# Kernel optimization log

Hardware: AMD Instinct MI355X
Metric: run time of the kernel (lower is better)

The kernel has to match this reference:

```python
import jax, jax.numpy as jnp
import numpy as np

N, E = 50000, 800000
DN, DE, H = 64, 32, 4
NODE_SCALE = float(np.sqrt(DN))
EDGE_SCALE = float(np.sqrt(DE))


def _linear_init(key, fan_in, fan_out):
    k1, k2 = jax.random.split(key)
    s = 1.0 / np.sqrt(fan_in)
    w = jax.random.uniform(k1, (fan_in, fan_out), minval=-s, maxval=s, dtype=jnp.float32)
    b = jax.random.uniform(k2, (fan_out,), minval=-s, maxval=s, dtype=jnp.float32)
    return w, b


def setup_inputs() -> dict:
    key = jax.random.key(0)
    ks = jax.random.split(key, 12)
    inp = {}
    inp['node_inputs'] = jax.random.normal(ks[0], (N, DN), dtype=jnp.float32)
    inp['edge_inputs'] = jax.random.normal(ks[1], (E, DE), dtype=jnp.float32)
    inp['src'] = jax.random.randint(ks[2], (E,), 0, N, dtype=jnp.int32)
    inp['dst'] = jax.random.randint(ks[3], (E,), 0, N, dtype=jnp.int32)
    # query / key MessageProjection params, value LinearProjection params
    specs = [('qn', DN, H * DN, ks[4]), ('qe', DE, H, ks[5]),
             ('kn', DN, H * DN, ks[6]), ('ke', DE, H, ks[7]),
             ('vn', DN, H * DN, ks[8]), ('ve', DE, H * DE, ks[9])]
    for name, fi, fo, k in specs:
        w, b = _linear_init(k, fi, fo)
        inp[name + '_w'] = w
        inp[name + '_b'] = b
    return inp


def _message_proj(x, e, src, dst, nw, nb, ew, eb):
    # node projection: relu(Linear) -> [N, H, DN]; edge weight: sigmoid(Linear) -> [E, H, 1]
    p = jax.nn.relu(x @ nw + nb).reshape(-1, H, DN)
    w = jax.nn.sigmoid(e @ ew + eb).reshape(-1, H, 1)
    msg = p[src] + w  # u_add_e -> [E, H, DN]
    ssum = jax.ops.segment_sum(msg, dst, num_segments=N)
    deg = jax.ops.segment_sum(jnp.ones((E, 1, 1), msg.dtype), dst, num_segments=N)
    agg = jnp.where(deg > 0, ssum / jnp.maximum(deg, 1.0), 0.0)  # mean reduce, 0 for isolated nodes
    return agg, w


def _attention(q, k, scale):
    # scores over heads: [*, H, H]; exp -> clamp(-5,5) -> softmax (matches torch order)
    s = jnp.clip(jnp.exp(jnp.einsum('nhd,ngd->nhg', q, k) / scale), -5.0, 5.0)
    return jax.nn.softmax(s, axis=-1)


def reference(node_inputs, edge_inputs, src, dst,
              qn_w, qn_b, qe_w, qe_b, kn_w, kn_b, ke_w, ke_b,
              vn_w, vn_b, ve_w, ve_b):
    node_q, edge_q = _message_proj(node_inputs, edge_inputs, src, dst, qn_w, qn_b, qe_w, qe_b)
    node_k, edge_k = _message_proj(node_inputs, edge_inputs, src, dst, kn_w, kn_b, ke_w, ke_b)
    node_v = jax.nn.relu(node_inputs @ vn_w + vn_b).reshape(-1, H, DN)
    edge_v = jax.nn.relu(edge_inputs @ ve_w + ve_b).reshape(-1, H, DE)
    node_attn = _attention(node_q, node_k, NODE_SCALE)  # [N, H, H]
    edge_attn = _attention(edge_q, edge_k, EDGE_SCALE)  # [E, H, H]
    node_emb = jnp.einsum('nhg,ngd->nhd', node_attn, node_v).mean(-2)  # [N, DN]
    edge_emb = jnp.einsum('ehg,egd->ehd', edge_attn, edge_v).mean(-2)  # [E, DE]
    return node_emb, edge_emb
```

## Files before the change

kernel.cpp:

```cpp
#include <hip/hip_runtime.h>
#include <math.h>

#define NN 50000
#define NE 800000

__device__ __forceinline__ unsigned bf16_2(float lo, float hi){
  unsigned a = __float_as_uint(lo), b = __float_as_uint(hi);
  unsigned ra = (a + 0x7fffu + ((a >> 16) & 1u)) >> 16;
  unsigned rb = (b + 0x7fffu + ((b >> 16) & 1u)) >> 16;
  return ra | (rb << 16);
}
__device__ __forceinline__ float bflo(unsigned u){ return __uint_as_float(u << 16); }
__device__ __forceinline__ float bfhi(unsigned u){ return __uint_as_float(u & 0xffff0000u); }

__global__ __launch_bounds__(256) void k_transpose_all(
    const float* __restrict__ qnw, const float* __restrict__ knw,
    const float* __restrict__ vnw, const float* __restrict__ vew,
    const float* __restrict__ qew, const float* __restrict__ kew,
    float* __restrict__ wqn, float* __restrict__ wkn, float* __restrict__ wvn,
    float* __restrict__ wve, float* __restrict__ wqe, float* __restrict__ wke){
  int b = blockIdx.x;
  const float* s; float* d; int R, C, base;
  if (b < 64)       { s = qnw; d = wqn; R = 64; C = 256; base = b; }
  else if (b < 128) { s = knw; d = wkn; R = 64; C = 256; base = b - 64; }
  else if (b < 192) { s = vnw; d = wvn; R = 64; C = 256; base = b - 128; }
  else if (b < 208) { s = vew; d = wve; R = 32; C = 128; base = b - 192; }
  else if (b == 208){ s = qew; d = wqe; R = 32; C = 4;   base = 0; }
  else              { s = kew; d = wke; R = 32; C = 4;   base = 0; }
  int idx = base * 256 + threadIdx.x;
  if (idx < R * C){
    int i = idx / C;
    int j = idx - i * C;
    d[j * R + i] = s[idx];
  }
}

__global__ __launch_bounds__(256) void k_node_proj(
    const float* __restrict__ x,
    const float* __restrict__ wtq, const float* __restrict__ bq,
    const float* __restrict__ wtk, const float* __restrict__ bk,
    const float* __restrict__ wtv, const float* __restrict__ bv,
    unsigned* __restrict__ pqk, float* __restrict__ pv){
  int n = blockIdx.x * 256 + threadIdx.x;
  if (n >= NN) return;
  int p = blockIdx.y;
  const float* wt = (p == 0) ? wtq : (p == 1) ? wtk : wtv;
  const float* bb = (p == 0) ? bq  : (p == 1) ? bk  : bv;
  float xs[64];
  const float4* xv = (const float4*)(x + (size_t)n * 64);
  #pragma unroll
  for (int i = 0; i < 16; i++){
    float4 t = xv[i];
    xs[4*i+0] = t.x; xs[4*i+1] = t.y; xs[4*i+2] = t.z; xs[4*i+3] = t.w;
  }
  for (int j4 = 0; j4 < 64; j4++){
    const float* w0 = wt + (size_t)j4 * 256;
    float a0 = bb[4*j4+0], a1 = bb[4*j4+1], a2 = bb[4*j4+2], a3 = bb[4*j4+3];
    #pragma unroll
    for (int c = 0; c < 64; c++){
      float xc = xs[c];
      a0 = fmaf(xc, w0[c],       a0);
      a1 = fmaf(xc, w0[64 + c],  a1);
      a2 = fmaf(xc, w0[128 + c], a2);
      a3 = fmaf(xc, w0[192 + c], a3);
    }
    a0 = fmaxf(a0, 0.f); a1 = fmaxf(a1, 0.f);
    a2 = fmaxf(a2, 0.f); a3 = fmaxf(a3, 0.f);
    if (p == 2){
      float4 o = { a0, a1, a2, a3 };
      *(float4*)(pv + (size_t)n * 256 + 4 * j4) = o;
    } else {
      uint2 o = { bf16_2(a0, a1), bf16_2(a2, a3) };
      *(uint2*)(pqk + (size_t)n * 256 + j4 * 4 + (p == 1 ? 2 : 0)) = o;
    }
  }
}

__device__ __forceinline__ void attn_mix(const float* dots, float inv_scale, float* cg){
  cg[0] = cg[1] = cg[2] = cg[3] = 0.f;
  #pragma unroll
  for (int h = 0; h < 4; h++){
    float sv[4], mx = -1e30f;
    #pragma unroll
    for (int g = 0; g < 4; g++){
      sv[g] = fminf(expf(dots[h*4 + g] * inv_scale), 5.f);
      mx = fmaxf(mx, sv[g]);
    }
    float rs = 0.f;
    #pragma unroll
    for (int g = 0; g < 4; g++){ sv[g] = expf(sv[g] - mx); rs += sv[g]; }
    float ir = 1.f / rs;
    #pragma unroll
    for (int g = 0; g < 4; g++) cg[g] += sv[g] * ir;
  }
  #pragma unroll
  for (int g = 0; g < 4; g++) cg[g] *= 0.25f;
}

__global__ __launch_bounds__(256) void k_edge_gate(
    const float* __restrict__ einp, const int* __restrict__ dstv,
    const float* __restrict__ qet, const float* __restrict__ qeb,
    const float* __restrict__ ket, const float* __restrict__ keb,
    int* __restrict__ counts, uint4* __restrict__ qwkw){
  int e = blockIdx.x * 256 + threadIdx.x;
  float es[32];
  const float4* ev4 = (const float4*)(einp + (size_t)e * 32);
  #pragma unroll
  for (int i = 0; i < 8; i++){
    float4 t = ev4[i];
    es[4*i+0] = t.x; es[4*i+1] = t.y; es[4*i+2] = t.z; es[4*i+3] = t.w;
  }
  float qw[4], kw[4];
  #pragma unroll
  for (int h = 0; h < 4; h++){
    float aq = qeb[h], ak = keb[h];
    #pragma unroll
    for (int c = 0; c < 32; c++){
      aq = fmaf(es[c], qet[h*32 + c], aq);
      ak = fmaf(es[c], ket[h*32 + c], ak);
    }
    qw[h] = 1.f / (1.f + expf(-aq));
    kw[h] = 1.f / (1.f + expf(-ak));
  }
  atomicAdd(&counts[dstv[e]], 1);
  uint4 o;
  o.x = bf16_2(qw[0], qw[1]);
  o.y = bf16_2(qw[2], qw[3]);
  o.z = bf16_2(kw[0], kw[1]);
  o.w = bf16_2(kw[2], kw[3]);
  qwkw[e] = o;
}

__global__ __launch_bounds__(256) void k_edge_gemm(
    const float* __restrict__ einp, const uint4* __restrict__ qwkw,
    const float* __restrict__ vet, const float* __restrict__ veb,
    float* __restrict__ edge_out){
  __shared__ float es_t[256 * 32];
  __shared__ float cg_t[256 * 4];
  int tid  = threadIdx.x;
  int wid  = tid >> 6;
  int lane = tid & 63;
  size_t blk_e = (size_t)blockIdx.x * 256;

  float w0[32], w1[32];
  {
    const float4* r0 = (const float4*)(vet + lane * 32);
    const float4* r1 = (const float4*)(vet + (lane + 64) * 32);
    #pragma unroll
    for (int i = 0; i < 8; i++){
      float4 a = r0[i], b = r1[i];
      w0[4*i+0]=a.x; w0[4*i+1]=a.y; w0[4*i+2]=a.z; w0[4*i+3]=a.w;
      w1[4*i+0]=b.x; w1[4*i+1]=b.y; w1[4*i+2]=b.z; w1[4*i+3]=b.w;
    }
  }
  float bias0 = veb[lane], bias1 = veb[lane + 64];

  const float4* src4 = (const float4*)(einp + blk_e * 32);
  float4* st4 = (float4*)es_t;
  #pragma unroll
  for (int r = 0; r < 8; r++) st4[r * 256 + tid] = src4[r * 256 + tid];
  {
    uint4 qk = qwkw[blk_e + tid];
    float qw[4] = { bflo(qk.x), bfhi(qk.x), bflo(qk.y), bfhi(qk.y) };
    float kw[4] = { bflo(qk.z), bfhi(qk.z), bflo(qk.w), bfhi(qk.w) };
    const float inv_scale = 0.17677669529663687f;
    float dots[16];
    #pragma unroll
    for (int h = 0; h < 4; h++)
      #pragma unroll
      for (int g = 0; g < 4; g++) dots[h*4 + g] = qw[h] * kw[g];
    float cg[4];
    attn_mix(dots, inv_scale, cg);
    float4 o = { cg[0], cg[1], cg[2], cg[3] };
    *(float4*)(cg_t + tid * 4) = o;
  }
  __syncthreads();

  int g0 = lane >> 5;
  for (int i0 = 0; i0 < 64; i0 += 2){
    int ea = wid * 64 + i0;
    const float4* xa4 = (const float4*)(es_t + ea * 32);
    const float4* xb4 = xa4 + 8;
    float a0 = bias0, a1 = bias1, c0 = bias0, c1 = bias1;
    #pragma unroll
    for (int c4 = 0; c4 < 8; c4++){
      float4 xa = xa4[c4], xb = xb4[c4];
      a0 = fmaf(xa.x, w0[4*c4+0], a0);
      a0 = fmaf(xa.y, w0[4*c4+1], a0);
      a0 = fmaf(xa.z, w0[4*c4+2], a0);
      a0 = fmaf(xa.w, w0[4*c4+3], a0);
      a1 = fmaf(xa.x, w1[4*c4+0], a1);
      a1 = fmaf(xa.y, w1[4*c4+1], a1);
      a1 = fmaf(xa.z, w1[4*c4+2], a1);
      a1 = fmaf(xa.w, w1[4*c4+3], a1);
      c0 = fmaf(xb.x, w0[4*c4+0], c0);
      c0 = fmaf(xb.y, w0[4*c4+1], c0);
      c0 = fmaf(xb.z, w0[4*c4+2], c0);
      c0 = fmaf(xb.w, w0[4*c4+3], c0);
      c1 = fmaf(xb.x, w1[4*c4+0], c1);
      c1 = fmaf(xb.y, w1[4*c4+1], c1);
      c1 = fmaf(xb.z, w1[4*c4+2], c1);
      c1 = fmaf(xb.w, w1[4*c4+3], c1);
    }
    float cga0 = cg_t[ea*4 + g0],       cga2 = cg_t[ea*4 + g0 + 2];
    float cgb0 = cg_t[(ea+1)*4 + g0],   cgb2 = cg_t[(ea+1)*4 + g0 + 2];
    float oa = cga0 * fmaxf(a0, 0.f) + cga2 * fmaxf(a1, 0.f);
    float ob = cgb0 * fmaxf(c0, 0.f) + cgb2 * fmaxf(c1, 0.f);
    oa += __shfl_xor(oa, 32, 64);
    ob += __shfl_xor(ob, 32, 64);
    float val = (lane < 32) ? oa : ob;
    edge_out[(blk_e + (size_t)ea) * 32 + lane] = val;
  }
}

__global__ __launch_bounds__(1024) void k_scan1(const int* __restrict__ counts,
                                                int* __restrict__ offsets,
                                                int* __restrict__ bsums){
  __shared__ int sd[1024];
  int tid = threadIdx.x;
  int gid = blockIdx.x * 1024 + tid;
  int v = (gid < NN) ? counts[gid] : 0;
  sd[tid] = v;
  __syncthreads();
  for (int off = 1; off < 1024; off <<= 1){
    int t = (tid >= off) ? sd[tid - off] : 0;
    __syncthreads();
    sd[tid] += t;
    __syncthreads();
  }
  int incl = sd[tid];
  if (gid < NN) offsets[gid] = incl - v;
  if (tid == 1023) bsums[blockIdx.x] = incl;
}

__global__ void k_scan2(int* __restrict__ bsums, int nb){
  int tid = threadIdx.x;
  int v = (tid < nb) ? bsums[tid] : 0;
  for (int off = 1; off < 64; off <<= 1){
    int t = __shfl_up(v, off, 64);
    if (tid >= off) v += t;
  }
  int ex = __shfl_up(v, 1, 64);
  if (tid == 0) ex = 0;
  if (tid < nb) bsums[tid] = ex;
}

__global__ __launch_bounds__(1024) void k_scan3(int* __restrict__ offsets,
                                                const int* __restrict__ bsums){
  int gid = blockIdx.x * 1024 + threadIdx.x;
  if (gid < NN) offsets[gid] += bsums[blockIdx.x];
  if (gid == 0) offsets[NN] = NE;
}

__global__ __launch_bounds__(256) void k_fill(
    const int* __restrict__ dstv, const int* __restrict__ srcv,
    const int* __restrict__ offsets, int* __restrict__ cursor,
    int2* __restrict__ csr2){
  int e = blockIdx.x * 256 + threadIdx.x;
  if (e >= NE) return;
  int d = dstv[e];
  int s = srcv[e];
  int pos = offsets[d] + atomicAdd(&cursor[d], 1);
  csr2[pos] = make_int2(e, s);
}

__global__ __launch_bounds__(256) void k_node_agg(
    const int* __restrict__ offsets, const int2* __restrict__ csr2,
    const uint4* __restrict__ qwkw, const uint4* __restrict__ pqk,
    const float* __restrict__ pv, float* __restrict__ node_out){
  __shared__ float tile[4][512];
  int wid  = threadIdx.x >> 6;
  int lane = threadIdx.x & 63;
  int n = blockIdx.x * 4 + wid;
  int off0 = offsets[n], off1 = offsets[n + 1];
  float4 qa = {0.f,0.f,0.f,0.f}, ka = {0.f,0.f,0.f,0.f};
  float qs0=0.f,qs1=0.f,qs2=0.f,qs3=0.f, ks0=0.f,ks1=0.f,ks2=0.f,ks3=0.f;
  int i = off0;
  while (i + 2 <= off1){
    int2 Ea = csr2[i], Eb = csr2[i + 1];
    uint4 ua = pqk[(size_t)Ea.y * 64 + lane];
    uint4 ub = pqk[(size_t)Eb.y * 64 + lane];
    uint4 ga = qwkw[Ea.x];
    uint4 gb = qwkw[Eb.x];
    qa.x += bflo(ua.x); qa.y += bfhi(ua.x); qa.z += bflo(ua.y); qa.w += bfhi(ua.y);
    ka.x += bflo(ua.z); ka.y += bfhi(ua.z); ka.z += bflo(ua.w); ka.w += bfhi(ua.w);
    qa.x += bflo(ub.x); qa.y += bfhi(ub.x); qa.z += bflo(ub.y); qa.w += bfhi(ub.y);
    ka.x += bflo(ub.z); ka.y += bfhi(ub.z); ka.z += bflo(ub.w); ka.w += bfhi(ub.w);
    qs0 += bflo(ga.x) + bflo(gb.x); qs1 += bfhi(ga.x) + bfhi(gb.x);
    qs2 += bflo(ga.y) + bflo(gb.y); qs3 += bfhi(ga.y) + bfhi(gb.y);
    ks0 += bflo(ga.z) + bflo(gb.z); ks1 += bfhi(ga.z) + bfhi(gb.z);
    ks2 += bflo(ga.w) + bflo(gb.w); ks3 += bfhi(ga.w) + bfhi(gb.w);
    i += 2;
  }
  if (i < off1){
    int2 Ea = csr2[i];
    uint4 ua = pqk[(size_t)Ea.y * 64 + lane];
    uint4 ga = qwkw[Ea.x];
    qa.x += bflo(ua.x); qa.y += bfhi(ua.x); qa.z += bflo(ua.y); qa.w += bfhi(ua.y);
    ka.x += bflo(ua.z); ka.y += bfhi(ua.z); ka.z += bflo(ua.w); ka.w += bfhi(ua.w);
    qs0 += bflo(ga.x); qs1 += bfhi(ga.x); qs2 += bflo(ga.y); qs3 += bfhi(ga.y);
    ks0 += bflo(ga.z); ks1 += bfhi(ga.z); ks2 += bflo(ga.w); ks3 += bfhi(ga.w);
  }
  float* tl = tile[wid];
  ((float4*)tl)[lane]      = qa;
  ((float4*)tl)[64 + lane] = ka;
  __syncthreads();
  float qh[4], kh[4];
  int deg = off1 - off0;
  float qsv[4] = { qs0, qs1, qs2, qs3 };
  float ksv[4] = { ks0, ks1, ks2, ks3 };
  if (deg > 0){
    float inv = 1.f / (float)deg;
    #pragma unroll
    for (int h = 0; h < 4; h++){
      qh[h] = (tl[h*64 + lane]       + qsv[h]) * inv;
      kh[h] = (tl[256 + h*64 + lane] + ksv[h]) * inv;
    }
  } else {
    #pragma unroll
    for (int h = 0; h < 4; h++){ qh[h] = 0.f; kh[h] = 0.f; }
  }
  float dots[16];
  #pragma unroll
  for (int h = 0; h < 4; h++)
    #pragma unroll
    for (int g = 0; g < 4; g++) dots[h*4 + g] = qh[h] * kh[g];
  #pragma unroll
  for (int m = 1; m < 64; m <<= 1){
    #pragma unroll
    for (int t = 0; t < 16; t++) dots[t] += __shfl_xor(dots[t], m, 64);
  }
  const float inv_ns = 0.125f;
  float cg[4];
  attn_mix(dots, inv_ns, cg);
  const float* vb = pv + (size_t)n * 256;
  float o = 0.f;
  #pragma unroll
  for (int g = 0; g < 4; g++) o = fmaf(cg[g], vb[g*64 + lane], o);
  node_out[(size_t)n * 64 + lane] = o;
}

extern "C" void kernel_launch(void* const* d_in, const int* in_sizes, int n_in,
                              void* d_out, int out_size, void* d_ws, size_t ws_size,
                              hipStream_t stream) {
  const float* node_inputs = (const float*)d_in[0];
  const float* edge_inputs = (const float*)d_in[1];
  const int*   srcv        = (const int*)d_in[2];
  const int*   dstv        = (const int*)d_in[3];
  const float* qn_w = (const float*)d_in[4];
  const float* qn_b = (const float*)d_in[5];
  const float* qe_w = (const float*)d_in[6];
  const float* qe_b = (const float*)d_in[7];
  const float* kn_w = (const float*)d_in[8];
  const float* kn_b = (const float*)d_in[9];
  const float* ke_w = (const float*)d_in[10];
  const float* ke_b = (const float*)d_in[11];
  const float* vn_w = (const float*)d_in[12];
  const float* vn_b = (const float*)d_in[13];
  const float* ve_w = (const float*)d_in[14];
  const float* ve_b = (const float*)d_in[15];

  float* out      = (float*)d_out;
  float* node_out = out;
  float* edge_out = out + (size_t)NN * 64;

  float* ws = (float*)d_ws;
  unsigned* pqk = (unsigned*)ws;
  float* pv     = (float*)(pqk + (size_t)NN * 256);
  uint4* qwkw   = (uint4*)(pv + (size_t)NN * 256);
  float* wt_qn  = (float*)(qwkw + NE);
  float* wt_kn  = wt_qn + 16384;
  float* wt_vn  = wt_kn + 16384;
  float* wt_ve  = wt_vn + 16384;
  float* wt_qe  = wt_ve + 4096;
  float* wt_ke  = wt_qe + 128;
  int* counts   = (int*)(wt_ke + 128);
  int* cursor   = counts + NN;
  int* offsets  = cursor + NN;
  int2* csr2    = (int2*)(offsets + NN + 2);
  int* bsums    = (int*)(csr2 + NE);

  hipMemsetAsync(counts, 0, (size_t)2 * NN * sizeof(int), stream);

  k_transpose_all<<<210, 256, 0, stream>>>(
      qn_w, kn_w, vn_w, ve_w, qe_w, ke_w,
      wt_qn, wt_kn, wt_vn, wt_ve, wt_qe, wt_ke);

  k_edge_gate<<<NE / 256, 256, 0, stream>>>(
      edge_inputs, dstv, wt_qe, qe_b, wt_ke, ke_b, counts, qwkw);
  k_edge_gemm<<<NE / 256, 256, 0, stream>>>(
      edge_inputs, qwkw, wt_ve, ve_b, edge_out);

  k_node_proj<<<dim3((NN + 255) / 256, 3), 256, 0, stream>>>(
      node_inputs, wt_qn, qn_b, wt_kn, kn_b, wt_vn, vn_b, pqk, pv);

  const int SB = (NN + 1023) / 1024;
  k_scan1<<<SB, 1024, 0, stream>>>(counts, offsets, bsums);
  k_scan2<<<1, 64, 0, stream>>>(bsums, SB);
  k_scan3<<<SB, 1024, 0, stream>>>(offsets, bsums);
  k_fill<<<NE / 256, 256, 0, stream>>>(dstv, srcv, offsets, cursor, csr2);

  k_node_agg<<<NN / 4, 256, 0, stream>>>(
      offsets, csr2, qwkw, (const uint4*)pqk, pv, node_out);
}
```

Baseline: 771.9 us.

## Split node projection into fused Q/K and separate V kernels with column tiling

Replaces the single node-projection kernel, which ran one block row per projection, with two kernels. The first computes Q and K together and writes each output as one 16-byte bf16 store, split across 4 column chunks in the grid. The second computes V split across 2 column chunks. The goal is more blocks in flight and shorter per-thread serial loops, at the cost of reloading each node's input row once per chunk and an extra kernel launch.

```diff
diff --git a/kernel.cpp b/kernel.cpp
--- a/kernel.cpp
+++ b/kernel.cpp
@@ -35,17 +35,14 @@
   }
 }
 
-__global__ __launch_bounds__(256) void k_node_proj(
+__global__ __launch_bounds__(256) void k_node_proj_qk(
     const float* __restrict__ x,
     const float* __restrict__ wtq, const float* __restrict__ bq,
     const float* __restrict__ wtk, const float* __restrict__ bk,
-    const float* __restrict__ wtv, const float* __restrict__ bv,
-    unsigned* __restrict__ pqk, float* __restrict__ pv){
+    unsigned* __restrict__ pqk){
   int n = blockIdx.x * 256 + threadIdx.x;
   if (n >= NN) return;
-  int p = blockIdx.y;
-  const float* wt = (p == 0) ? wtq : (p == 1) ? wtk : wtv;
-  const float* bb = (p == 0) ? bq  : (p == 1) ? bk  : bv;
+  int j0 = blockIdx.y * 16;
   float xs[64];
   const float4* xv = (const float4*)(x + (size_t)n * 64);
   #pragma unroll
@@ -53,9 +50,49 @@
     float4 t = xv[i];
     xs[4*i+0] = t.x; xs[4*i+1] = t.y; xs[4*i+2] = t.z; xs[4*i+3] = t.w;
   }
-  for (int j4 = 0; j4 < 64; j4++){
-    const float* w0 = wt + (size_t)j4 * 256;
-    float a0 = bb[4*j4+0], a1 = bb[4*j4+1], a2 = bb[4*j4+2], a3 = bb[4*j4+3];
+  for (int j4 = j0; j4 < j0 + 16; j4++){
+    const float* wq = wtq + (size_t)j4 * 256;
+    const float* wk = wtk + (size_t)j4 * 256;
+    float a0 = bq[4*j4+0], a1 = bq[4*j4+1], a2 = bq[4*j4+2], a3 = bq[4*j4+3];
+    float c0 = bk[4*j4+0], c1 = bk[4*j4+1], c2 = bk[4*j4+2], c3 = bk[4*j4+3];
+    #pragma unroll
+    for (int c = 0; c < 64; c++){
+      float xc = xs[c];
+      a0 = fmaf(xc, wq[c],       a0);
+      a1 = fmaf(xc, wq[64 + c],  a1);
+      a2 = fmaf(xc, wq[128 + c], a2);
+      a3 = fmaf(xc, wq[192 + c], a3);
+      c0 = fmaf(xc, wk[c],       c0);
+      c1 = fmaf(xc, wk[64 + c],  c1);
+      c2 = fmaf(xc, wk[128 + c], c2);
+      c3 = fmaf(xc, wk[192 + c], c3);
+    }
+    a0 = fmaxf(a0, 0.f); a1 = fmaxf(a1, 0.f);
+    a2 = fmaxf(a2, 0.f); a3 = fmaxf(a3, 0.f);
+    c0 = fmaxf(c0, 0.f); c1 = fmaxf(c1, 0.f);
+    c2 = fmaxf(c2, 0.f); c3 = fmaxf(c3, 0.f);
+    uint4 o = { bf16_2(a0, a1), bf16_2(a2, a3), bf16_2(c0, c1), bf16_2(c2, c3) };
+    *(uint4*)(pqk + (size_t)n * 256 + j4 * 4) = o;
+  }
+}
+
+__global__ __launch_bounds__(256) void k_node_proj_v(
+    const float* __restrict__ x,
+    const float* __restrict__ wtv, const float* __restrict__ bv,
+    float* __restrict__ pv){
+  int n = blockIdx.x * 256 + threadIdx.x;
+  if (n >= NN) return;
+  int j0 = blockIdx.y * 32;
+  float xs[64];
+  const float4* xv = (const float4*)(x + (size_t)n * 64);
+  #pragma unroll
+  for (int i = 0; i < 16; i++){
+    float4 t = xv[i];
+    xs[4*i+0] = t.x; xs[4*i+1] = t.y; xs[4*i+2] = t.z; xs[4*i+3] = t.w;
+  }
+  for (int j4 = j0; j4 < j0 + 32; j4++){
+    const float* w0 = wtv + (size_t)j4 * 256;
+    float a0 = bv[4*j4+0], a1 = bv[4*j4+1], a2 = bv[4*j4+2], a3 = bv[4*j4+3];
     #pragma unroll
     for (int c = 0; c < 64; c++){
       float xc = xs[c];
@@ -64,15 +101,8 @@
       a2 = fmaf(xc, w0[128 + c], a2);
       a3 = fmaf(xc, w0[192 + c], a3);
     }
-    a0 = fmaxf(a0, 0.f); a1 = fmaxf(a1, 0.f);
-    a2 = fmaxf(a2, 0.f); a3 = fmaxf(a3, 0.f);
-    if (p == 2){
-      float4 o = { a0, a1, a2, a3 };
-      *(float4*)(pv + (size_t)n * 256 + 4 * j4) = o;
-    } else {
-      uint2 o = { bf16_2(a0, a1), bf16_2(a2, a3) };
-      *(uint2*)(pqk + (size_t)n * 256 + j4 * 4 + (p == 1 ? 2 : 0)) = o;
-    }
+    float4 o = { fmaxf(a0, 0.f), fmaxf(a1, 0.f), fmaxf(a2, 0.f), fmaxf(a3, 0.f) };
+    *(float4*)(pv + (size_t)n * 256 + 4 * j4) = o;
   }
 }
 
@@ -391,8 +421,10 @@
   k_edge_gemm<<<NE / 256, 256, 0, stream>>>(
       edge_inputs, qwkw, wt_ve, ve_b, edge_out);
 
-  k_node_proj<<<dim3((NN + 255) / 256, 3), 256, 0, stream>>>(
-      node_inputs, wt_qn, qn_b, wt_kn, kn_b, wt_vn, vn_b, pqk, pv);
+  k_node_proj_qk<<<dim3((NN + 255) / 256, 4), 256, 0, stream>>>(
+      node_inputs, wt_qn, qn_b, wt_kn, kn_b, pqk);
+  k_node_proj_v<<<dim3((NN + 255) / 256, 2), 256, 0, stream>>>(
+      node_inputs, wt_vn, vn_b, pv);
 
   const int SB = (NN + 1023) / 1024;
   k_scan1<<<SB, 1024, 0, stream>>>(counts, offsets, bsums);
```

New measurement: 812.2 us. 1.05x slower.
